# Kernel tuning notes

Hardware: AMD Instinct MI355X
Metric: run time of the kernel (lower is better)

Reference implementation:

```python
import jax, jax.numpy as jnp
import numpy as np

N_NODES = 50000
NEG_SLOPE = 0.2  # PyG GATConv default leaky_relu slope


def gat_conv(x, src, dst, W, a_src, a_dst, b):
    """One PyG-style GATConv (concat heads, add_self_loops already applied).
    x: [N, F_in]; W: [H*C, F_in]; a_src/a_dst: [H, C]; b: [H*C]."""
    N = x.shape[0]
    H, C = a_src.shape
    h = (x @ W.T).reshape(N, H, C)                       # [N,H,C]
    alpha_src = jnp.einsum('nhc,hc->nh', h, a_src)       # [N,H]
    alpha_dst = jnp.einsum('nhc,hc->nh', h, a_dst)       # [N,H]
    e = alpha_src[src] + alpha_dst[dst]                  # [E,H]
    e = jax.nn.leaky_relu(e, NEG_SLOPE)
    # segment softmax over incoming edges of each dst node, per head
    m = jax.ops.segment_max(e, dst, num_segments=N)      # [N,H]
    w = jnp.exp(e - m[dst])                              # [E,H]
    s = jax.ops.segment_sum(w, dst, num_segments=N)      # [N,H]
    alpha = w / (s[dst] + 1e-16)                         # [E,H]
    msg = alpha[:, :, None] * h[src]                     # [E,H,C]
    out = jax.ops.segment_sum(msg, dst, num_segments=N)  # [N,H,C]
    return out.reshape(N, H * C) + b


def setup_inputs() -> dict:
    key = jax.random.key(0)
    ks = jax.random.split(key, 8)
    N, E, F_in, H, C, L = N_NODES, 800000, 128, 4, 32, 3
    x = jax.random.normal(ks[0], (N, F_in), dtype=jnp.float32)
    edge_index = jax.random.randint(ks[1], (2, E), 0, N, dtype=jnp.int32)
    Ws = jax.random.normal(ks[2], (L, H * C, F_in), dtype=jnp.float32) * 0.1
    att_src = jax.random.normal(ks[3], (L, H, C), dtype=jnp.float32) * 0.1
    att_dst = jax.random.normal(ks[4], (L, H, C), dtype=jnp.float32) * 0.1
    conv_bias = jnp.zeros((L, H * C), dtype=jnp.float32)
    Wf = jax.random.normal(ks[5], (32, H * C), dtype=jnp.float32) * 0.1
    bf = jnp.zeros((32,), dtype=jnp.float32)
    return {"x": x, "Ws": Ws, "att_src": att_src, "att_dst": att_dst,
            "conv_bias": conv_bias, "Wf": Wf, "bf": bf, "edge_index": edge_index}


def reference(x, Ws, att_src, att_dst, conv_bias, Wf, bf, edge_index):
    N = x.shape[0]
    # PyG GATConv add_self_loops=True (default): append i->i for every node
    loop = jnp.arange(N, dtype=edge_index.dtype)
    src = jnp.concatenate([edge_index[0], loop])
    dst = jnp.concatenate([edge_index[1], loop])
    for l in range(Ws.shape[0]):
        x = gat_conv(x, src, dst, Ws[l], att_src[l], att_dst[l], conv_bias[l])
        x = jax.nn.relu(x)
        # F.dropout(p=0.1, training=False) is identity in eval mode
    return x @ Wf.T + bf
```

## Files before the change

kernel.cpp:

```cpp
#include <hip/hip_runtime.h>
#include <hip/hip_bf16.h>
#include <math.h>

#define N_NODES 50000
#define NE      800000
#define ETOT    (NE + N_NODES)
#define F       128
#define NHEAD   4
#define NEG     0.2f

#define CAP 64
#define GM 64
#define GGEMM ((N_NODES + GM - 1) / GM)
#define GBUILD ((ETOT + 255) / 256)

typedef __attribute__((ext_vector_type(8))) short bf16x8;
typedef __attribute__((ext_vector_type(4))) float f32x4;
typedef _Float16 f16x8 __attribute__((ext_vector_type(8)));


__device__ __forceinline__ unsigned short f2bf(float x) {
    unsigned int u = __float_as_uint(x);
    u += 0x7FFFu + ((u >> 16) & 1u);
    return (unsigned short)(u >> 16);
}
__device__ __forceinline__ float bf2f(unsigned short h) {
    return __uint_as_float(((unsigned int)h) << 16);
}
__device__ __forceinline__ void cvt8(float4 a, float4 b, bf16x8* hi, bf16x8* lo) {
    float f[8] = {a.x, a.y, a.z, a.w, b.x, b.y, b.z, b.w};
    bf16x8 h, l;
#pragma unroll
    for (int j = 0; j < 8; j++) {
        unsigned short hu = f2bf(f[j]);
        h[j] = (short)hu;
        l[j] = (short)f2bf(f[j] - bf2f(hu));
    }
    *hi = h; *lo = l;
}
__device__ __forceinline__ void cvt8h(float4 a, float4 b, f16x8* hi, f16x8* lo) {
    float f[8] = {a.x, a.y, a.z, a.w, b.x, b.y, b.z, b.w};
    f16x8 h, l;
#pragma unroll
    for (int j = 0; j < 8; j++) {
        _Float16 hh = (_Float16)f[j];
        h[j] = hh;
        l[j] = (_Float16)(f[j] - (float)hh);
    }
    *hi = h; *lo = l;
}

__device__ __forceinline__ int lds_unit(int m, int q) {
    return 4 * m + (q ^ ((m >> 1) & 3));
}


__global__ __launch_bounds__(256) void k_gemm_build(
        const float* __restrict__ X,
        const float* __restrict__ W,
        const float* __restrict__ a_s,
        const float* __restrict__ a_d,
        _Float16* __restrict__ hout,
        float* __restrict__ asrc,
        float* __restrict__ adst,
        const int* __restrict__ ei,
        int* __restrict__ deg,
        int* __restrict__ col) {
    __shared__ short Ah[256 * 8], Al[256 * 8];
    __shared__ short Bh[512 * 8], Bl[512 * 8];
    int tid = threadIdx.x;

    if (blockIdx.x >= GGEMM) {
        int i = (blockIdx.x - GGEMM) * 256 + tid;
        if (i < ETOT) {
            int s, d;
            if (i < NE) { s = ei[i]; d = ei[NE + i]; }
            else        { s = i - NE; d = s; }
            int r = atomicAdd(&deg[d], 1);
            if (r < CAP) col[d * CAP + r] = s;
        }
        return;
    }

    int bm = blockIdx.x * GM;

    int am = tid >> 2, aq = tid & 3;
    int xunit = ((am >> 4) << 6) + lds_unit(am & 15, aq);
    int wj = tid >> 2, wq = tid & 3;
    int wunit = ((wj >> 4) << 6) + lds_unit(wj & 15, wq);

    int lane = tid & 63, wv = tid >> 6;
    int fm = lane & 15, fq = lane >> 4;
    int a_unit = (wv << 6) + lds_unit(fm, fq);
    int b_unit0 = lds_unit(fm, fq);

    f32x4 acc[8];
#pragma unroll
    for (int nt = 0; nt < 8; nt++) acc[nt] = (f32x4){0.f, 0.f, 0.f, 0.f};

    float4 xp0, xp1, wp0, wp1, wp2, wp3;
    int gr = bm + am;
    bool xok = (gr < N_NODES);
    const float* xrow = X + (size_t)gr * F + aq * 8;
    const float* wrow1 = W + (size_t)wj * F + wq * 8;
    const float* wrow2 = W + (size_t)(wj + 64) * F + wq * 8;
    float4 z4 = make_float4(0.f, 0.f, 0.f, 0.f);

    auto load_tile = [&](int k0) {
        xp0 = xok ? *(const float4*)(xrow + k0)     : z4;
        xp1 = xok ? *(const float4*)(xrow + k0 + 4) : z4;
        wp0 = *(const float4*)(wrow1 + k0);
        wp1 = *(const float4*)(wrow1 + k0 + 4);
        wp2 = *(const float4*)(wrow2 + k0);
        wp3 = *(const float4*)(wrow2 + k0 + 4);
    };
    auto store_tile = [&]() {
        bf16x8 hi, lo;
        cvt8(xp0, xp1, &hi, &lo);
        *(bf16x8*)&Ah[xunit * 8] = hi;  *(bf16x8*)&Al[xunit * 8] = lo;
        cvt8(wp0, wp1, &hi, &lo);
        *(bf16x8*)&Bh[wunit * 8] = hi;  *(bf16x8*)&Bl[wunit * 8] = lo;
        cvt8(wp2, wp3, &hi, &lo);
        *(bf16x8*)&Bh[(wunit + 256) * 8] = hi;  *(bf16x8*)&Bl[(wunit + 256) * 8] = lo;
    };

    load_tile(0);
    store_tile();
    __syncthreads();

#pragma unroll
    for (int t = 0; t < 4; t++) {
        if (t < 3) load_tile((t + 1) * 32);
        bf16x8 ah = *(bf16x8*)&Ah[a_unit * 8];
        bf16x8 al = *(bf16x8*)&Al[a_unit * 8];
#pragma unroll
        for (int nt = 0; nt < 8; nt++) {
            int bu = ((nt << 6) + b_unit0) * 8;
            bf16x8 bh = *(bf16x8*)&Bh[bu];
            bf16x8 bl = *(bf16x8*)&Bl[bu];
            acc[nt] = __builtin_amdgcn_mfma_f32_16x16x32_bf16(ah, bh, acc[nt], 0, 0, 0);
            acc[nt] = __builtin_amdgcn_mfma_f32_16x16x32_bf16(ah, bl, acc[nt], 0, 0, 0);
            acc[nt] = __builtin_amdgcn_mfma_f32_16x16x32_bf16(al, bh, acc[nt], 0, 0, 0);
        }
        __syncthreads();
        if (t < 3) { store_tile(); __syncthreads(); }
    }

    float as_v[8], ad_v[8];
#pragma unroll
    for (int nt = 0; nt < 8; nt++) {
        as_v[nt] = a_s[nt * 16 + fm];
        ad_v[nt] = a_d[nt * 16 + fm];
    }
#pragma unroll
    for (int r = 0; r < 4; r++) {
        int n = bm + wv * 16 + fq * 4 + r;
        bool ok = (n < N_NODES);
        if (ok) {
#pragma unroll
            for (int nt = 0; nt < 8; nt++)
                hout[(size_t)n * F + nt * 16 + fm] = (_Float16)acc[nt][r];
        }
        float ps[4], pd[4];
#pragma unroll
        for (int hh = 0; hh < 4; hh++) {
            ps[hh] = acc[2 * hh][r] * as_v[2 * hh] + acc[2 * hh + 1][r] * as_v[2 * hh + 1];
            pd[hh] = acc[2 * hh][r] * ad_v[2 * hh] + acc[2 * hh + 1][r] * ad_v[2 * hh + 1];
        }
#pragma unroll
        for (int s = 1; s < 16; s <<= 1) {
#pragma unroll
            for (int hh = 0; hh < 4; hh++) {
                ps[hh] += __shfl_xor(ps[hh], s);
                pd[hh] += __shfl_xor(pd[hh], s);
            }
        }
        if (ok && fm == 0) {
            *(float4*)&asrc[n * 4] = make_float4(ps[0], ps[1], ps[2], ps[3]);
            *(float4*)&adst[n * 4] = make_float4(pd[0], pd[1], pd[2], pd[3]);
        }
    }
}


__global__ __launch_bounds__(256) void k_gemm16(const _Float16* __restrict__ X,
                                                const float* __restrict__ W,
                                                const float* __restrict__ a_s,
                                                const float* __restrict__ a_d,
                                                _Float16* __restrict__ hout,
                                                float* __restrict__ asrc,
                                                float* __restrict__ adst) {
    __shared__ _Float16 Ahf[256 * 8];
    __shared__ _Float16 Bhf[512 * 8], Blf[512 * 8];
    int tid = threadIdx.x;
    int bm = blockIdx.x * GM;

    int am = tid >> 2, aq = tid & 3;
    int xunit = ((am >> 4) << 6) + lds_unit(am & 15, aq);
    int wj = tid >> 2, wq = tid & 3;
    int wunit = ((wj >> 4) << 6) + lds_unit(wj & 15, wq);

    int lane = tid & 63, wv = tid >> 6;
    int fm = lane & 15, fq = lane >> 4;
    int a_unit = (wv << 6) + lds_unit(fm, fq);
    int b_unit0 = lds_unit(fm, fq);

    f32x4 acc[8];
#pragma unroll
    for (int nt = 0; nt < 8; nt++) acc[nt] = (f32x4){0.f, 0.f, 0.f, 0.f};

    f16x8 xp;
    float4 wp0, wp1, wp2, wp3;
    int gr = bm + am;
    bool xok = (gr < N_NODES);
    const _Float16* xrow = X + (size_t)gr * F + aq * 8;
    const float* wrow1 = W + (size_t)wj * F + wq * 8;
    const float* wrow2 = W + (size_t)(wj + 64) * F + wq * 8;

    auto load_tile = [&](int k0) {
        f16x8 zz = {0, 0, 0, 0, 0, 0, 0, 0};
        xp = xok ? *(const f16x8*)(xrow + k0) : zz;
        wp0 = *(const float4*)(wrow1 + k0);
        wp1 = *(const float4*)(wrow1 + k0 + 4);
        wp2 = *(const float4*)(wrow2 + k0);
        wp3 = *(const float4*)(wrow2 + k0 + 4);
    };
    auto store_tile = [&]() {
        *(f16x8*)&Ahf[xunit * 8] = xp;
        f16x8 hi, lo;
        cvt8h(wp0, wp1, &hi, &lo);
        *(f16x8*)&Bhf[wunit * 8] = hi;  *(f16x8*)&Blf[wunit * 8] = lo;
        cvt8h(wp2, wp3, &hi, &lo);
        *(f16x8*)&Bhf[(wunit + 256) * 8] = hi;  *(f16x8*)&Blf[(wunit + 256) * 8] = lo;
    };

    load_tile(0);
    store_tile();
    __syncthreads();

#pragma unroll
    for (int t = 0; t < 4; t++) {
        if (t < 3) load_tile((t + 1) * 32);
        f16x8 ah = *(f16x8*)&Ahf[a_unit * 8];
#pragma unroll
        for (int nt = 0; nt < 8; nt++) {
            int bu = ((nt << 6) + b_unit0) * 8;
            f16x8 bh = *(f16x8*)&Bhf[bu];
            f16x8 bl = *(f16x8*)&Blf[bu];
            acc[nt] = __builtin_amdgcn_mfma_f32_16x16x32_f16(ah, bh, acc[nt], 0, 0, 0);
            acc[nt] = __builtin_amdgcn_mfma_f32_16x16x32_f16(ah, bl, acc[nt], 0, 0, 0);
        }
        __syncthreads();
        if (t < 3) { store_tile(); __syncthreads(); }
    }

    float as_v[8], ad_v[8];
#pragma unroll
    for (int nt = 0; nt < 8; nt++) {
        as_v[nt] = a_s[nt * 16 + fm];
        ad_v[nt] = a_d[nt * 16 + fm];
    }
#pragma unroll
    for (int r = 0; r < 4; r++) {
        int n = bm + wv * 16 + fq * 4 + r;
        bool ok = (n < N_NODES);
        if (ok) {
#pragma unroll
            for (int nt = 0; nt < 8; nt++)
                hout[(size_t)n * F + nt * 16 + fm] = (_Float16)acc[nt][r];
        }
        float ps[4], pd[4];
#pragma unroll
        for (int hh = 0; hh < 4; hh++) {
            ps[hh] = acc[2 * hh][r] * as_v[2 * hh] + acc[2 * hh + 1][r] * as_v[2 * hh + 1];
            pd[hh] = acc[2 * hh][r] * ad_v[2 * hh] + acc[2 * hh + 1][r] * ad_v[2 * hh + 1];
        }
#pragma unroll
        for (int s = 1; s < 16; s <<= 1) {
#pragma unroll
            for (int hh = 0; hh < 4; hh++) {
                ps[hh] += __shfl_xor(ps[hh], s);
                pd[hh] += __shfl_xor(pd[hh], s);
            }
        }
        if (ok && fm == 0) {
            *(float4*)&asrc[n * 4] = make_float4(ps[0], ps[1], ps[2], ps[3]);
            *(float4*)&adst[n * 4] = make_float4(pd[0], pd[1], pd[2], pd[3]);
        }
    }
}


#define EPAD 68

__global__ __launch_bounds__(256) void k_aggr(const _Float16* __restrict__ h,
                                              const float* __restrict__ asrc,
                                              const float* __restrict__ adst,
                                              const int* __restrict__ deg,
                                              const int* __restrict__ col,
                                              const float* __restrict__ bias,
                                              _Float16* __restrict__ xout) {
    __shared__ int   scol[4][64];
    __shared__ float swT[4][4 * EPAD];
    int wave = threadIdx.x >> 6;
    int lane = threadIdx.x & 63;
    int n = blockIdx.x * 4 + wave;
    if (n >= N_NODES) return;
    int wl = lane & 15;
    int he = lane >> 4;
    int hc = wl >> 2;
    int cnt = deg[n]; if (cnt > CAP) cnt = CAP;
    int beg = n * CAP;
    float4 ad4 = *(const float4*)&adst[n * 4];

    float s_run = 0.f;
    float acc[8];
#pragma unroll
    for (int j = 0; j < 8; j++) acc[j] = 0.f;

    {
        int sidx = 0;
        float4 w4 = make_float4(0.f, 0.f, 0.f, 0.f);
        if (lane < cnt) {
            sidx = col[beg + lane];
            float4 av = *(const float4*)&asrc[sidx * 4];
            float ex = av.x + ad4.x, ey = av.y + ad4.y,
                  ez = av.z + ad4.z, ew = av.w + ad4.w;
            ex = (ex > 0.f) ? ex : NEG * ex;
            ey = (ey > 0.f) ? ey : NEG * ey;
            ez = (ez > 0.f) ? ez : NEG * ez;
            ew = (ew > 0.f) ? ew : NEG * ew;
            w4.x = __expf(ex); w4.y = __expf(ey);
            w4.z = __expf(ez); w4.w = __expf(ew);
        }
        scol[wave][lane] = sidx;
        swT[wave][0 * EPAD + lane] = w4.x;
        swT[wave][1 * EPAD + lane] = w4.y;
        swT[wave][2 * EPAD + lane] = w4.z;
        swT[wave][3 * EPAD + lane] = w4.w;
        __builtin_amdgcn_sched_barrier(0);
        float4 wv4 = *(float4*)&swT[wave][he * EPAD + wl * 4];
        float S = (wv4.x + wv4.y) + (wv4.z + wv4.w);
#pragma unroll
        for (int s = 1; s < 16; s <<= 1) S += __shfl_xor(S, s);
        s_run += S;
        __builtin_amdgcn_sched_barrier(0);
#pragma unroll 2
        for (int p = 0; p < cnt; p += 4) {
            int ep = p + he;
            int s = scol[wave][ep];
            float wgt = swT[wave][hc * EPAD + ep];
            f16x8 hv = *(const f16x8*)&h[(size_t)s * F + wl * 8];
#pragma unroll
            for (int j = 0; j < 8; j++)
                acc[j] = fmaf(wgt, (float)hv[j], acc[j]);
        }
    }

#pragma unroll
    for (int j = 0; j < 8; j++) {
        acc[j] += __shfl_xor(acc[j], 16);
        acc[j] += __shfl_xor(acc[j], 32);
    }
    float sv = __shfl(s_run, hc * 16);
    float inv = 1.f / (sv + 1e-16f);
    float4 b0 = *(const float4*)&bias[wl * 8];
    float4 b1 = *(const float4*)&bias[wl * 8 + 4];
    float bb[8] = {b0.x, b0.y, b0.z, b0.w, b1.x, b1.y, b1.z, b1.w};
    if (he == 0) {
        f16x8 st;
#pragma unroll
        for (int j = 0; j < 8; j++)
            st[j] = (_Float16)fmaxf(fmaf(acc[j], inv, bb[j]), 0.f);
        *(f16x8*)&xout[(size_t)n * F + wl * 8] = st;
    }
}


#define FCB 128

__global__ __launch_bounds__(256) void k_fc(const _Float16* __restrict__ X,
                                            const float* __restrict__ Wf,
                                            const float* __restrict__ bf,
                                            float* __restrict__ out) {
    __shared__ float WsT[128 * 36];
    __shared__ float XsT[32 * 132];
    int tid = threadIdx.x;
    int bm = blockIdx.x * FCB;

#pragma unroll
    for (int u = 0; u < 16; u++) {
        int idx = tid + 256 * u;
        int o = idx & 31, k = idx >> 5;
        WsT[k * 36 + o] = Wf[o * 128 + k];
    }

    int tx = tid & 7;
    int ty = tid >> 3;
    float acc[4][4];
#pragma unroll
    for (int i = 0; i < 4; i++)
#pragma unroll
        for (int j = 0; j < 4; j++) acc[i][j] = 0.f;

    for (int k0 = 0; k0 < 128; k0 += 32) {
        __syncthreads();
#pragma unroll
        for (int u = 0; u < 2; u++) {
            int idx = tid + 256 * u;
            int nn = idx & 127, c = idx >> 7;
            int gn = bm + nn;
            f16x8 v = {0, 0, 0, 0, 0, 0, 0, 0};
            if (gn < N_NODES) v = *(const f16x8*)&X[(size_t)gn * F + k0 + c * 8];
#pragma unroll
            for (int j = 0; j < 8; j++)
                XsT[(c * 8 + j) * 132 + nn] = (float)v[j];
        }
        __syncthreads();

#pragma unroll
        for (int kk = 0; kk < 32; kk++) {
            float4 xv = *(float4*)&XsT[kk * 132 + ty * 4];
            float4 wv = *(float4*)&WsT[(k0 + kk) * 36 + tx * 4];
            float xs[4] = {xv.x, xv.y, xv.z, xv.w};
            float ws[4] = {wv.x, wv.y, wv.z, wv.w};
#pragma unroll
            for (int i = 0; i < 4; i++)
#pragma unroll
                for (int j = 0; j < 4; j++)
                    acc[i][j] = fmaf(xs[i], ws[j], acc[i][j]);
        }
    }

    float4 bv = *(const float4*)&bf[tx * 4];
#pragma unroll
    for (int i = 0; i < 4; i++) {
        int n = bm + ty * 4 + i;
        if (n < N_NODES) {
            float4 o4 = make_float4(acc[i][0] + bv.x, acc[i][1] + bv.y,
                                    acc[i][2] + bv.z, acc[i][3] + bv.w);
            *(float4*)&out[n * 32 + tx * 4] = o4;
        }
    }
}


extern "C" void kernel_launch(void* const* d_in, const int* in_sizes, int n_in,
                              void* d_out, int out_size, void* d_ws, size_t ws_size,
                              hipStream_t stream) {
    const float* x      = (const float*)d_in[0];
    const float* Ws     = (const float*)d_in[1];
    const float* a_src  = (const float*)d_in[2];
    const float* a_dst  = (const float*)d_in[3];
    const float* cbias  = (const float*)d_in[4];
    const float* Wf     = (const float*)d_in[5];
    const float* bf     = (const float*)d_in[6];
    const int*   ei     = (const int*)d_in[7];
    float* out = (float*)d_out;

    char* p = (char*)d_ws;
    auto carve = [&](size_t bytes) {
        char* r = p;
        p += (bytes + 255) & ~(size_t)255;
        return r;
    };
    _Float16* xA   = (_Float16*)carve((size_t)N_NODES * F * 2);
    _Float16* xB   = (_Float16*)carve((size_t)N_NODES * F * 2);
    _Float16* xC   = (_Float16*)carve((size_t)N_NODES * F * 2);
    _Float16* hbuf = (_Float16*)carve((size_t)N_NODES * F * 2);
    float* asrc = (float*)carve((size_t)N_NODES * NHEAD * 4);
    float* adst = (float*)carve((size_t)N_NODES * NHEAD * 4);
    int* deg    = (int*)carve((size_t)N_NODES * 4);
    int* col    = (int*)carve((size_t)N_NODES * CAP * 4);

    int gaggr = (N_NODES + 3) / 4;

    hipMemsetAsync(deg, 0, (size_t)N_NODES * 4, stream);
    k_gemm_build<<<GGEMM + GBUILD, 256, 0, stream>>>(
        x, Ws, a_src, a_dst, hbuf, asrc, adst, ei, deg, col);
    k_aggr<<<gaggr, 256, 0, stream>>>(hbuf, asrc, adst, deg, col, cbias, xA);

    k_gemm16<<<GGEMM, 256, 0, stream>>>(xA, Ws + (size_t)F * F, a_src + F, a_dst + F,
                                        hbuf, asrc, adst);
    k_aggr<<<gaggr, 256, 0, stream>>>(hbuf, asrc, adst, deg, col, cbias + F, xB);

    k_gemm16<<<GGEMM, 256, 0, stream>>>(xB, Ws + (size_t)2 * F * F, a_src + 2 * F,
                                        a_dst + 2 * F, hbuf, asrc, adst);
    k_aggr<<<gaggr, 256, 0, stream>>>(hbuf, asrc, adst, deg, col, cbias + 2 * F, xC);

    k_fc<<<(N_NODES + FCB - 1) / FCB, 256, 0, stream>>>(xC, Wf, bf, out);
}
```

Before: 327.8 us.

## Build CSR adjacency via two-pass LDS bucketing instead of global atomics

Replaces the per-edge global atomicAdd scatter into a fixed-capacity adjacency list with a two-phase build. First, 256 partition blocks bucket their edge chunk by destination high bits using LDS atomics and write packed (dst<<16|src) words. Then a placement kernel per 256-node bucket builds the column list with shared atomics and appends the self loop. This removes heavy contention on global atomics and the deg memset, at the cost of an extra kernel launch. Packing src into 16 bits truncates node ids at or above 65536, which is safe only for N=50000, and the per-partition SUBCAP of 64 may drop edges.

```diff
diff --git a/kernel.cpp b/kernel.cpp
--- a/kernel.cpp
+++ b/kernel.cpp
@@ -4,7 +4,6 @@
 
 #define N_NODES 50000
 #define NE      800000
-#define ETOT    (NE + N_NODES)
 #define F       128
 #define NHEAD   4
 #define NEG     0.2f
@@ -12,7 +11,11 @@
 #define CAP 64
 #define GM 64
 #define GGEMM ((N_NODES + GM - 1) / GM)
-#define GBUILD ((ETOT + 255) / 256)
+
+#define NPART  256
+#define ECHUNK ((NE + NPART - 1) / NPART)
+#define NBKT   ((N_NODES + 255) / 256)
+#define SUBCAP 64
 
 typedef __attribute__((ext_vector_type(8))) short bf16x8;
 typedef __attribute__((ext_vector_type(4))) float f32x4;
@@ -55,7 +58,7 @@
 }
 
 
-__global__ __launch_bounds__(256) void k_gemm_build(
+__global__ __launch_bounds__(256) void k_gemm_part(
         const float* __restrict__ X,
         const float* __restrict__ W,
         const float* __restrict__ a_s,
@@ -64,25 +67,33 @@
         float* __restrict__ asrc,
         float* __restrict__ adst,
         const int* __restrict__ ei,
-        int* __restrict__ deg,
-        int* __restrict__ col) {
+        unsigned int* __restrict__ bkt,
+        int* __restrict__ cnt2) {
     __shared__ short Ah[256 * 8], Al[256 * 8];
     __shared__ short Bh[512 * 8], Bl[512 * 8];
+    __shared__ int pcnt[NBKT];
     int tid = threadIdx.x;
 
-    if (blockIdx.x >= GGEMM) {
-        int i = (blockIdx.x - GGEMM) * 256 + tid;
-        if (i < ETOT) {
-            int s, d;
-            if (i < NE) { s = ei[i]; d = ei[NE + i]; }
-            else        { s = i - NE; d = s; }
-            int r = atomicAdd(&deg[d], 1);
-            if (r < CAP) col[d * CAP + r] = s;
-        }
+    if (blockIdx.x < NPART) {
+        int blk = blockIdx.x;
+        if (tid < NBKT) pcnt[tid] = 0;
+        __syncthreads();
+        int start = blk * ECHUNK;
+        int end = start + ECHUNK; if (end > NE) end = NE;
+        for (int i = start + tid; i < end; i += 256) {
+            unsigned s = (unsigned)ei[i];
+            unsigned d = (unsigned)ei[NE + i];
+            int b = (int)(d >> 8);
+            int r = atomicAdd(&pcnt[b], 1);
+            if (r < SUBCAP)
+                bkt[(size_t)(b * NPART + blk) * SUBCAP + r] = (d << 16) | s;
+        }
+        __syncthreads();
+        if (tid < NBKT) cnt2[tid * NPART + blk] = pcnt[tid];
         return;
     }
 
-    int bm = blockIdx.x * GM;
+    int bm = (blockIdx.x - NPART) * GM;
 
     int am = tid >> 2, aq = tid & 3;
     int xunit = ((am >> 4) << 6) + lds_unit(am & 15, aq);
@@ -179,6 +190,35 @@
             *(float4*)&asrc[n * 4] = make_float4(ps[0], ps[1], ps[2], ps[3]);
             *(float4*)&adst[n * 4] = make_float4(pd[0], pd[1], pd[2], pd[3]);
         }
+    }
+}
+
+
+__global__ __launch_bounds__(256) void k_place(const unsigned int* __restrict__ bkt,
+                                               const int* __restrict__ cnt2,
+                                               int* __restrict__ deg,
+                                               int* __restrict__ col) {
+    __shared__ int cnt[256];
+    int b = blockIdx.x;
+    int t = threadIdx.x;
+    cnt[t] = 0;
+    __syncthreads();
+    int c = cnt2[b * NPART + t];
+    if (c > SUBCAP) c = SUBCAP;
+    const unsigned int* seg = bkt + (size_t)(b * NPART + t) * SUBCAP;
+    for (int j = 0; j < c; j++) {
+        unsigned int e = seg[j];
+        int d = (int)(e >> 16), s = (int)(e & 0xFFFFu);
+        int r = atomicAdd(&cnt[d & 255], 1);
+        if (r < CAP - 1) col[d * CAP + r] = s;
+    }
+    __syncthreads();
+    int node = (b << 8) + t;
+    if (node < N_NODES) {
+        int r = cnt[t];
+        if (r > CAP - 1) r = CAP - 1;
+        col[node * CAP + r] = node;
+        deg[node] = r + 1;
     }
 }
 
@@ -472,12 +512,14 @@
     float* adst = (float*)carve((size_t)N_NODES * NHEAD * 4);
     int* deg    = (int*)carve((size_t)N_NODES * 4);
     int* col    = (int*)carve((size_t)N_NODES * CAP * 4);
+    unsigned int* bkt = (unsigned int*)carve((size_t)NBKT * NPART * SUBCAP * 4);
+    int* cnt2   = (int*)carve((size_t)NBKT * NPART * 4);
 
     int gaggr = (N_NODES + 3) / 4;
 
-    hipMemsetAsync(deg, 0, (size_t)N_NODES * 4, stream);
-    k_gemm_build<<<GGEMM + GBUILD, 256, 0, stream>>>(
-        x, Ws, a_src, a_dst, hbuf, asrc, adst, ei, deg, col);
+    k_gemm_part<<<NPART + GGEMM, 256, 0, stream>>>(
+        x, Ws, a_src, a_dst, hbuf, asrc, adst, ei, bkt, cnt2);
+    k_place<<<NBKT, 256, 0, stream>>>(bkt, cnt2, deg, col);
     k_aggr<<<gaggr, 256, 0, stream>>>(hbuf, asrc, adst, deg, col, cbias, xA);
 
     k_gemm16<<<GGEMM, 256, 0, stream>>>(xA, Ws + (size_t)F * F, a_src + F, a_dst + F,
```

Result: faster. 277.2 us (-15.4%).
